# Performance work log

Hardware: AMD Instinct MI355X
Metric: run time of the kernel (lower is better)

The kernel has to match this reference:

```python
import jax, jax.numpy as jnp
import numpy as np

N_NODES = 100000
N_EDGES = 3200000
NUM_GRAPHS = 512
D_IN, D_H = 7, 16


def gcn_conv(x, edge_index, W, b, n_nodes):
    # PyG GCNConv: x' = D^{-1/2} (A + I) D^{-1/2} X W + b
    h = x @ W  # [N, d_out] -- do the tiny GEMM first (fewer bytes moved per edge)
    row, col = edge_index[0], edge_index[1]  # messages flow row -> col
    loop = jnp.arange(n_nodes)
    row = jnp.concatenate([row, loop])
    col = jnp.concatenate([col, loop])
    deg = jax.ops.segment_sum(jnp.ones(row.shape[0], dtype=h.dtype), col,
                              num_segments=n_nodes)
    dinv = jnp.where(deg > 0, jax.lax.rsqrt(deg), 0.0)
    norm = dinv[row] * dinv[col]                      # [E+N]
    msg = h[row] * norm[:, None]                      # gather + scale
    out = jax.ops.segment_sum(msg, col, num_segments=n_nodes)  # scatter-add
    return out + b


def setup_inputs() -> dict:
    key = jax.random.key(0)
    ks = jax.random.split(key, 9)
    x = jax.random.normal(ks[0], (N_NODES, D_IN), dtype=jnp.float32)
    edge_index = jax.random.randint(ks[1], (2, N_EDGES), 0, N_NODES, dtype=jnp.int64)
    batch = jnp.sort(jax.random.randint(ks[2], (N_NODES,), 0, NUM_GRAPHS, dtype=jnp.int64))
    def glorot(k, fan_in, fan_out):
        lim = np.sqrt(6.0 / (fan_in + fan_out)).astype(np.float32)
        return jax.random.uniform(k, (fan_in, fan_out), jnp.float32, -lim, lim)
    return {
        "x": x, "edge_index": edge_index, "batch": batch,
        "W1": glorot(ks[3], D_IN, D_H), "b1": jnp.zeros((D_H,), jnp.float32),
        "W2": glorot(ks[4], D_H, D_H), "b2": jnp.zeros((D_H,), jnp.float32),
        "Wl": glorot(ks[5], D_H, 1),   "bl": jnp.zeros((1,), jnp.float32),
    }


def reference(x, edge_index, batch, W1, b1, W2, b2, Wl, bl):
    n = x.shape[0]
    h = jax.nn.relu(gcn_conv(x, edge_index, W1, b1, n))
    h = jax.nn.relu(gcn_conv(h, edge_index, W2, b2, n))
    # global_mean_pool over graphs
    sums = jax.ops.segment_sum(h, batch, num_segments=NUM_GRAPHS)
    cnts = jax.ops.segment_sum(jnp.ones((n,), h.dtype), batch, num_segments=NUM_GRAPHS)
    pooled = sums / jnp.maximum(cnts, 1.0)[:, None]   # [G, 16]
    out = jax.nn.sigmoid(pooled @ Wl + bl)            # [G, 1]
    return out.squeeze(1)                             # [G]
```

## Files before the change

kernel.cpp:

```cpp
#include <hip/hip_runtime.h>
#include <hip/hip_fp16.h>
#include <math.h>

#define N_NODES    100000
#define N_EDGES    3200000
#define NUM_GRAPHS 512
#define D_IN       7
#define D_H        16
#define D_H2       8
#define SHIFT      7
#define BWIDTH     128
#define NB         782
#define CHUNK      8192
#define NCH        391
#define PC         2
#define PB         2
#define TPH        36
#define HST        (8 * TPH)
#define TP1        36
#define HST1       (4 * TP1)

__global__ void hist_kernel(const int* __restrict__ col, int* __restrict__ cnt) {
    __shared__ int lh[NB];
    int tid = threadIdx.x;
    for (int i = tid; i < NB; i += blockDim.x) lh[i] = 0;
    __syncthreads();
    int e0 = blockIdx.x * CHUNK;
    int e1 = e0 + CHUNK; if (e1 > N_EDGES) e1 = N_EDGES;
    for (int e = e0 + tid; e < e1; e += blockDim.x)
        atomicAdd(&lh[col[e] >> SHIFT], 1);
    __syncthreads();
    int* outp = cnt + (size_t)blockIdx.x * NB;
    for (int i = tid; i < NB; i += blockDim.x) outp[i] = lh[i];
}

__global__ void colscan_kernel(const int* __restrict__ cnt, int* __restrict__ base,
                               int* __restrict__ bcnt) {
    __shared__ int ts[256];
    int b = blockIdx.x;
    int tid = threadIdx.x;
    int c0 = tid * PC;
    int vals[PC];
    int sum = 0;
#pragma unroll
    for (int q = 0; q < PC; ++q) {
        int c = c0 + q;
        int v = (c < NCH) ? cnt[(size_t)c * NB + b] : 0;
        vals[q] = v; sum += v;
    }
    ts[tid] = sum;
    __syncthreads();
    for (int st = 1; st < 256; st <<= 1) {
        int v = (tid >= st) ? ts[tid - st] : 0;
        __syncthreads();
        ts[tid] += v;
        __syncthreads();
    }
    int run = ts[tid] - sum;
    int* bp = base + (size_t)b * NCH;
#pragma unroll
    for (int q = 0; q < PC; ++q) {
        int c = c0 + q;
        if (c < NCH) { bp[c] = run; run += vals[q]; }
    }
    if (tid == 0) bcnt[b] = ts[255];
}

__global__ void scan_kernel(const int* __restrict__ bcnt, int* __restrict__ offs) {
    __shared__ int lds[1024];
    int tid = threadIdx.x;
    lds[tid] = (tid < NB) ? bcnt[tid] : 0;
    __syncthreads();
    for (int st = 1; st < 1024; st <<= 1) {
        int v = (tid >= st) ? lds[tid - st] : 0;
        __syncthreads();
        lds[tid] += v;
        __syncthreads();
    }
    if (tid < NB) offs[tid + 1] = lds[tid];
    if (tid == 0) offs[0] = 0;
}

__global__ void place_kernel(const int* __restrict__ row, const int* __restrict__ col,
                             const int* __restrict__ base, const int* __restrict__ offs,
                             int* __restrict__ part) {
    __shared__ int lh[NB];
    __shared__ int sc[NB];
    __shared__ int lb[NB];
    __shared__ int ts[512];
    __shared__ int stage[CHUNK];
    __shared__ int dstv[CHUNK];

    int c = blockIdx.x;
    int tid = threadIdx.x;
    int e0 = c * CHUNK;
    int e1 = e0 + CHUNK; if (e1 > N_EDGES) e1 = N_EDGES;
    int n  = e1 - e0;

    for (int i = tid; i < NB; i += blockDim.x) lh[i] = 0;
    __syncthreads();
    for (int e = e0 + tid; e < e1; e += blockDim.x)
        atomicAdd(&lh[col[e] >> SHIFT], 1);
    __syncthreads();
    int b0 = tid * PB;
    int vals[PB];
    int sum = 0;
#pragma unroll
    for (int q = 0; q < PB; ++q) {
        int b = b0 + q;
        int v = (b < NB) ? lh[b] : 0;
        vals[q] = v; sum += v;
    }
    ts[tid] = sum;
    __syncthreads();
    for (int st = 1; st < 512; st <<= 1) {
        int v = (tid >= st) ? ts[tid - st] : 0;
        __syncthreads();
        ts[tid] += v;
        __syncthreads();
    }
    int run = ts[tid] - sum;
#pragma unroll
    for (int q = 0; q < PB; ++q) {
        int b = b0 + q;
        if (b < NB) {
            sc[b] = run;
            lb[b] = offs[b] + base[(size_t)b * NCH + c];
            run += vals[q];
            lh[b] = 0;
        }
    }
    __syncthreads();
    for (int e = e0 + tid; e < e1; e += blockDim.x) {
        int cc = col[e];
        int b = cc >> SHIFT;
        int rank = atomicAdd(&lh[b], 1);
        int loc = sc[b] + rank;
        stage[loc] = (row[e] << SHIFT) | (cc & (BWIDTH - 1));
        dstv[loc]  = lb[b] + rank;
    }
    __syncthreads();
    for (int i = tid; i < n; i += blockDim.x)
        part[dstv[i]] = stage[i];
}

__global__ void csr_kernel(const int* __restrict__ part, const int* __restrict__ offs,
                           const float* __restrict__ x,
                           int* __restrict__ csr, int* __restrict__ node_off,
                           int* __restrict__ deg, float* __restrict__ dinv,
                           unsigned* __restrict__ xsh) {
    __shared__ int cnt[BWIDTH];
    __shared__ int scn[BWIDTH];
    __shared__ int cur[BWIDTH];
    int b = blockIdx.x;
    int o0 = offs[b], o1 = offs[b + 1];
    if (threadIdx.x < BWIDTH) cnt[threadIdx.x] = 0;
    __syncthreads();
    for (int j = o0 + threadIdx.x; j < o1; j += blockDim.x)
        atomicAdd(&cnt[part[j] & (BWIDTH - 1)], 1);
    __syncthreads();
    if (threadIdx.x < BWIDTH) scn[threadIdx.x] = cnt[threadIdx.x];
    __syncthreads();
    for (int st = 1; st < BWIDTH; st <<= 1) {
        int v = 0;
        if (threadIdx.x < BWIDTH && threadIdx.x >= st) v = scn[threadIdx.x - st];
        __syncthreads();
        if (threadIdx.x < BWIDTH) scn[threadIdx.x] += v;
        __syncthreads();
    }
    if (threadIdx.x < BWIDTH) {
        int excl = scn[threadIdx.x] - cnt[threadIdx.x];
        cur[threadIdx.x] = excl;
        int c = b * BWIDTH + threadIdx.x;
        if (c < N_NODES) {
            node_off[c] = o0 + excl;
            deg[c] = cnt[threadIdx.x];
            float dv = rsqrtf((float)cnt[threadIdx.x] + 1.0f);
            dinv[c] = dv;
            float xv[8];
#pragma unroll
            for (int j = 0; j < D_IN; ++j) xv[j] = x[(size_t)c * D_IN + j] * dv;
            xv[7] = 0.f;
#pragma unroll
            for (int w = 0; w < 4; ++w) {
                __half2 p = __floats2half2_rn(xv[2 * w], xv[2 * w + 1]);
                xsh[(size_t)c * 4 + w] = *(unsigned*)&p;
            }
        }
    }
    __syncthreads();
    for (int j = o0 + threadIdx.x; j < o1; j += blockDim.x) {
        int e = part[j];
        int l = e & (BWIDTH - 1);
        int pos = atomicAdd(&cur[l], 1);
        csr[o0 + pos] = e >> SHIFT;
    }
}

__global__ void __launch_bounds__(256, 8)
pull1_kernel(const unsigned* __restrict__ xsh, const int* __restrict__ csr,
             const int* __restrict__ node_off, const int* __restrict__ deg,
             const float* __restrict__ dinv, const float* __restrict__ b1,
             const float* __restrict__ W1, const float* __restrict__ W2,
             unsigned* __restrict__ s2h) {
    __shared__ unsigned stage[4][2 * HST1];
    __shared__ float aggrow[4][2][8];
    __shared__ float hrow[4][2][D_H];
    int wave = threadIdx.x >> 6;
    int lane = threadIdx.x & 63;
    int h = lane >> 5, l = lane & 31;
    int v = blockIdx.x * 8 + wave * 2 + h;
    int k = l & 15;
    float w1c[D_IN];
#pragma unroll
    for (int j = 0; j < D_IN; ++j) w1c[j] = W1[j * D_H + k];
    float w2c[D_H];
#pragma unroll
    for (int j = 0; j < D_H; ++j) w2c[j] = W2[j * D_H + k];
    int d = deg[v], o0 = node_off[v];
    unsigned* stg = stage[wave] + h * HST1;
    int rg = l >> 3, p = l & 7;
    int w = p >> 1;
    bool hi = (p & 1);
    const uint4* rp = (const uint4*)(stg + w * TP1 + rg * 8);
    float acc = 0.f;
    for (int base = 0; base < d; base += 32) {
        int j = base + l;
        uint4 a = make_uint4(0u, 0u, 0u, 0u);
        if (j < d) {
            int r = __builtin_nontemporal_load(&csr[o0 + j]);
            a = *(const uint4*)(xsh + (size_t)r * 4);
        }
        asm volatile("s_waitcnt lgkmcnt(0)" ::: "memory");
        stg[0 * TP1 + l] = a.x;
        stg[1 * TP1 + l] = a.y;
        stg[2 * TP1 + l] = a.z;
        stg[3 * TP1 + l] = a.w;
        asm volatile("s_waitcnt lgkmcnt(0)" ::: "memory");
        uint4 q0 = rp[0], q1 = rp[1];
        unsigned ws[8] = { q0.x, q0.y, q0.z, q0.w, q1.x, q1.y, q1.z, q1.w };
#pragma unroll
        for (int i = 0; i < 8; ++i) {
            __half2 ph = *(__half2*)&ws[i];
            acc += hi ? __high2float(ph) : __low2float(ph);
        }
    }
    acc += __shfl_xor(acc, 8, 64);
    acc += __shfl_xor(acc, 16, 64);
    float dv = dinv[v];
    if (l < 8) aggrow[wave][h][l] = acc;
    asm volatile("s_waitcnt lgkmcnt(0)" ::: "memory");
    uint4 sx = *(const uint4*)(xsh + (size_t)v * 4);
    unsigned sxw[4] = { sx.x, sx.y, sx.z, sx.w };
    const float* ag = aggrow[wave][h];
    float hv = b1[k];
#pragma unroll
    for (int j = 0; j < D_IN; ++j) {
        __half2 ph = *(__half2*)&sxw[j >> 1];
        float xsv = (j & 1) ? __high2float(ph) : __low2float(ph);
        hv += dv * (ag[j] + xsv) * w1c[j];
    }
    hv = fmaxf(hv, 0.f);
    if (l < 16) hrow[wave][h][k] = hv;
    asm volatile("s_waitcnt lgkmcnt(0)" ::: "memory");
    const float4* hp = (const float4*)hrow[wave][h];
    float4 h0 = hp[0], h1 = hp[1], h2 = hp[2], h3 = hp[3];
    float a2 = h0.x * w2c[0] + h0.y * w2c[1] + h0.z * w2c[2] + h0.w * w2c[3]
             + h1.x * w2c[4] + h1.y * w2c[5] + h1.z * w2c[6] + h1.w * w2c[7]
             + h2.x * w2c[8] + h2.y * w2c[9] + h2.z * w2c[10] + h2.w * w2c[11]
             + h3.x * w2c[12] + h3.y * w2c[13] + h3.z * w2c[14] + h3.w * w2c[15];
    a2 *= dv;
    float a2hi = __shfl_xor(a2, 1, 64);
    if (l < 16 && (k & 1) == 0) {
        __half2 pq = __floats2half2_rn(a2, a2hi);
        s2h[(size_t)v * D_H2 + (k >> 1)] = *(unsigned*)&pq;
    }
}

__device__ __forceinline__ float gather_half(const unsigned* __restrict__ sh,
                                             const int* __restrict__ csr,
                                             int o0, int d, unsigned* stg, int l) {
    int g = l >> 4, k = l & 15;
    const uint4* rp = (const uint4*)(stg + (k >> 1) * TPH + g * 16);
    bool hi = (k & 1);
    float acc = 0.f;
    for (int base = 0; base < d; base += 32) {
        int j = base + l;
        uint4 a = make_uint4(0u, 0u, 0u, 0u), b = make_uint4(0u, 0u, 0u, 0u);
        if (j < d) {
            int r = __builtin_nontemporal_load(&csr[o0 + j]);
            const uint4* sp = (const uint4*)(sh + (size_t)r * D_H2);
            a = sp[0];
            b = sp[1];
        }
        asm volatile("s_waitcnt lgkmcnt(0)" ::: "memory");
        stg[0 * TPH + l] = a.x;
        stg[1 * TPH + l] = a.y;
        stg[2 * TPH + l] = a.z;
        stg[3 * TPH + l] = a.w;
        stg[4 * TPH + l] = b.x;
        stg[5 * TPH + l] = b.y;
        stg[6 * TPH + l] = b.z;
        stg[7 * TPH + l] = b.w;
        asm volatile("s_waitcnt lgkmcnt(0)" ::: "memory");
        uint4 q0 = rp[0], q1 = rp[1], q2 = rp[2], q3 = rp[3];
        unsigned ws[16] = { q0.x, q0.y, q0.z, q0.w, q1.x, q1.y, q1.z, q1.w,
                            q2.x, q2.y, q2.z, q2.w, q3.x, q3.y, q3.z, q3.w };
#pragma unroll
        for (int i = 0; i < 16; ++i) {
            __half2 p = *(__half2*)&ws[i];
            acc += hi ? __high2float(p) : __low2float(p);
        }
    }
    acc += __shfl_xor(acc, 16, 64);
    return acc;
}

__global__ void __launch_bounds__(256, 8)
pull2_kernel(const unsigned* __restrict__ sh, const int* __restrict__ csr,
             const int* __restrict__ node_off, const int* __restrict__ deg,
             const float* __restrict__ dinv, const float* __restrict__ b2,
             float* __restrict__ h2) {
    __shared__ unsigned stage[4][2 * HST];
    int wave = threadIdx.x >> 6;
    int lane = threadIdx.x & 63;
    int h = lane >> 5, l = lane & 31;
    int v = blockIdx.x * 8 + wave * 2 + h;
    int k = l & 15;
    int d = deg[v], o0 = node_off[v];
    unsigned* stg = stage[wave] + h * HST;
    float acc = gather_half(sh, csr, o0, d, stg, l);
    if (l < 16) {
        float dv = dinv[v];
        unsigned ws = sh[(size_t)v * D_H2 + (k >> 1)];
        __half2 ps = *(__half2*)&ws;
        float selfv = (k & 1) ? __high2float(ps) : __low2float(ps);
        float o = dv * (acc + selfv) + b2[k];
        h2[(size_t)v * D_H + k] = fmaxf(o, 0.f);
    }
}

__global__ void pool_head_kernel(const float* __restrict__ h, const int* __restrict__ batch,
                                 const float* __restrict__ Wl, const float* __restrict__ bl,
                                 float* __restrict__ out) {
    int g = blockIdx.x;
    int lo = 0, hi = N_NODES;
    while (lo < hi) { int m = (lo + hi) >> 1; if (batch[m] < g) lo = m + 1; else hi = m; }
    int v0 = lo;
    int lo2 = v0, hi2 = N_NODES;
    while (lo2 < hi2) { int m = (lo2 + hi2) >> 1; if (batch[m] < g + 1) lo2 = m + 1; else hi2 = m; }
    int v1 = lo2;
    int k = threadIdx.x & 15;
    int vi = threadIdx.x >> 4;
    float acc = 0.f;
    for (int v = v0 + vi; v < v1; v += 16) acc += h[v * D_H + k];
    acc += __shfl_xor(acc, 16, 64);
    acc += __shfl_xor(acc, 32, 64);
    __shared__ float sm[4][D_H];
    int lane = threadIdx.x & 63;
    if (lane < 16) sm[threadIdx.x >> 6][k] = acc;
    __syncthreads();
    if (threadIdx.x < 16) {
        float tot = sm[0][k] + sm[1][k] + sm[2][k] + sm[3][k];
        float cntf = (float)(v1 - v0);
        tot /= fmaxf(cntf, 1.0f);
        float p = tot * Wl[k];
        p += __shfl_xor(p, 1, 64);
        p += __shfl_xor(p, 2, 64);
        p += __shfl_xor(p, 4, 64);
        p += __shfl_xor(p, 8, 64);
        if (k == 0) out[g] = 1.0f / (1.0f + expf(-(p + bl[0])));
    }
}


extern "C" void kernel_launch(void* const* d_in, const int* in_sizes, int n_in,
                              void* d_out, int out_size, void* d_ws, size_t ws_size,
                              hipStream_t stream) {
    const float* x     = (const float*)d_in[0];
    const int*   ei    = (const int*)d_in[1];
    const int*   batch = (const int*)d_in[2];
    const float* W1    = (const float*)d_in[3];
    const float* b1    = (const float*)d_in[4];
    const float* W2    = (const float*)d_in[5];
    const float* b2    = (const float*)d_in[6];
    const float* Wl    = (const float*)d_in[7];
    const float* bl    = (const float*)d_in[8];
    float* out = (float*)d_out;

    const int* row = ei;
    const int* col = ei + N_EDGES;

    char* wsb = (char*)d_ws;
    size_t o = 0;
    int*      part     = (int*)(wsb + o);      o += (size_t)N_EDGES * 4;
    char*     regionA  = wsb + o;              o += (size_t)N_EDGES * 4;
    int*      cnt      = (int*)regionA;
    int*      base     = (int*)(regionA + (size_t)NCH * NB * 4);
    int*      csr      = (int*)regionA;
    int*      bcnt     = (int*)(wsb + o);      o += 1024 * 4;
    int*      offs     = (int*)(wsb + o);      o += 1024 * 4;
    int*      node_off = (int*)(wsb + o);      o += 100352 * 4;
    int*      deg      = (int*)(wsb + o);      o += 100352 * 4;
    float*    dinv     = (float*)(wsb + o);    o += 100352 * 4;
    unsigned* xsh      = (unsigned*)(wsb + o); o += (size_t)N_NODES * 4 * 4;
    unsigned* sBh      = (unsigned*)(wsb + o); o += (size_t)N_NODES * D_H2 * 4;
    float*    h2       = (float*)(wsb + o);    o += (size_t)N_NODES * D_H * 4;

    const int B = 256;

    hist_kernel<<<NCH, 512, 0, stream>>>(col, cnt);
    colscan_kernel<<<NB, B, 0, stream>>>(cnt, base, bcnt);
    scan_kernel<<<1, 1024, 0, stream>>>(bcnt, offs);
    place_kernel<<<NCH, 512, 0, stream>>>(row, col, base, offs, part);
    csr_kernel<<<NB, 512, 0, stream>>>(part, offs, x, csr, node_off, deg, dinv, xsh);

    pull1_kernel<<<N_NODES / 8, B, 0, stream>>>(xsh, csr, node_off, deg, dinv,
                                                b1, W1, W2, sBh);
    pull2_kernel<<<N_NODES / 8, B, 0, stream>>>(sBh, csr, node_off, deg, dinv,
                                                b2, h2);
    pool_head_kernel<<<NUM_GRAPHS, B, 0, stream>>>(h2, batch, Wl, bl, out);
}
```

Before: 134.9 us.

## Sort nodes by degree, prefetch next edge batch, vectorize edge index loads

Adds a degree histogram and a counting-sort permutation so the pull kernels process nodes grouped by similar degree, which evens out the per-wave work. Both pull kernels now software-prefetch the next 32-edge batch of neighbor features while the current batch is staged and reduced, hiding gather latency. The hist and place kernels read col/row as int4 vectors, which assumes the edge count is divisible by 4 per chunk. Costs are two extra small kernels, a memset, and more register pressure from the prefetch.

```diff
diff --git a/kernel.cpp b/kernel.cpp
--- a/kernel.cpp
+++ b/kernel.cpp
@@ -26,9 +26,16 @@
     for (int i = tid; i < NB; i += blockDim.x) lh[i] = 0;
     __syncthreads();
     int e0 = blockIdx.x * CHUNK;
-    int e1 = e0 + CHUNK; if (e1 > N_EDGES) e1 = N_EDGES;
-    for (int e = e0 + tid; e < e1; e += blockDim.x)
-        atomicAdd(&lh[col[e] >> SHIFT], 1);
+    int n  = N_EDGES - e0; if (n > CHUNK) n = CHUNK;
+    const int4* cp = (const int4*)(col + e0);
+    int n4 = n >> 2;
+    for (int q = tid; q < n4; q += blockDim.x) {
+        int4 v = cp[q];
+        atomicAdd(&lh[v.x >> SHIFT], 1);
+        atomicAdd(&lh[v.y >> SHIFT], 1);
+        atomicAdd(&lh[v.z >> SHIFT], 1);
+        atomicAdd(&lh[v.w >> SHIFT], 1);
+    }
     __syncthreads();
     int* outp = cnt + (size_t)blockIdx.x * NB;
     for (int i = tid; i < NB; i += blockDim.x) outp[i] = lh[i];
@@ -94,13 +101,20 @@
     int c = blockIdx.x;
     int tid = threadIdx.x;
     int e0 = c * CHUNK;
-    int e1 = e0 + CHUNK; if (e1 > N_EDGES) e1 = N_EDGES;
-    int n  = e1 - e0;
+    int n  = N_EDGES - e0; if (n > CHUNK) n = CHUNK;
+    int n4 = n >> 2;
+    const int4* cp = (const int4*)(col + e0);
+    const int4* rp = (const int4*)(row + e0);
 
     for (int i = tid; i < NB; i += blockDim.x) lh[i] = 0;
     __syncthreads();
-    for (int e = e0 + tid; e < e1; e += blockDim.x)
-        atomicAdd(&lh[col[e] >> SHIFT], 1);
+    for (int q = tid; q < n4; q += blockDim.x) {
+        int4 v = cp[q];
+        atomicAdd(&lh[v.x >> SHIFT], 1);
+        atomicAdd(&lh[v.y >> SHIFT], 1);
+        atomicAdd(&lh[v.z >> SHIFT], 1);
+        atomicAdd(&lh[v.w >> SHIFT], 1);
+    }
     __syncthreads();
     int b0 = tid * PB;
     int vals[PB];
@@ -131,13 +145,20 @@
         }
     }
     __syncthreads();
-    for (int e = e0 + tid; e < e1; e += blockDim.x) {
-        int cc = col[e];
-        int b = cc >> SHIFT;
-        int rank = atomicAdd(&lh[b], 1);
-        int loc = sc[b] + rank;
-        stage[loc] = (row[e] << SHIFT) | (cc & (BWIDTH - 1));
-        dstv[loc]  = lb[b] + rank;
+    for (int q = tid; q < n4; q += blockDim.x) {
+        int4 cc4 = cp[q];
+        int4 rr4 = rp[q];
+        int ccs[4] = { cc4.x, cc4.y, cc4.z, cc4.w };
+        int rrs[4] = { rr4.x, rr4.y, rr4.z, rr4.w };
+#pragma unroll
+        for (int t = 0; t < 4; ++t) {
+            int cc = ccs[t];
+            int b = cc >> SHIFT;
+            int rank = atomicAdd(&lh[b], 1);
+            int loc = sc[b] + rank;
+            stage[loc] = (rrs[t] << SHIFT) | (cc & (BWIDTH - 1));
+            dstv[loc]  = lb[b] + rank;
+        }
     }
     __syncthreads();
     for (int i = tid; i < n; i += blockDim.x)
@@ -148,13 +169,14 @@
                            const float* __restrict__ x,
                            int* __restrict__ csr, int* __restrict__ node_off,
                            int* __restrict__ deg, float* __restrict__ dinv,
-                           unsigned* __restrict__ xsh) {
+                           unsigned* __restrict__ xsh, int* __restrict__ dcnt) {
     __shared__ int cnt[BWIDTH];
     __shared__ int scn[BWIDTH];
     __shared__ int cur[BWIDTH];
+    __shared__ int dh[128];
     int b = blockIdx.x;
     int o0 = offs[b], o1 = offs[b + 1];
-    if (threadIdx.x < BWIDTH) cnt[threadIdx.x] = 0;
+    if (threadIdx.x < BWIDTH) { cnt[threadIdx.x] = 0; dh[threadIdx.x] = 0; }
     __syncthreads();
     for (int j = o0 + threadIdx.x; j < o1; j += blockDim.x)
         atomicAdd(&cnt[part[j] & (BWIDTH - 1)], 1);
@@ -175,6 +197,8 @@
         if (c < N_NODES) {
             node_off[c] = o0 + excl;
             deg[c] = cnt[threadIdx.x];
+            int bin = cnt[threadIdx.x]; if (bin > 127) bin = 127;
+            atomicAdd(&dh[bin], 1);
             float dv = rsqrtf((float)cnt[threadIdx.x] + 1.0f);
             dinv[c] = dv;
             float xv[8];
@@ -189,6 +213,7 @@
         }
     }
     __syncthreads();
+    if (threadIdx.x < 128 && dh[threadIdx.x]) atomicAdd(&dcnt[threadIdx.x], dh[threadIdx.x]);
     for (int j = o0 + threadIdx.x; j < o1; j += blockDim.x) {
         int e = part[j];
         int l = e & (BWIDTH - 1);
@@ -197,19 +222,52 @@
     }
 }
 
+__global__ void dscan_kernel(const int* __restrict__ dcnt, int* __restrict__ dcur) {
+    __shared__ int s[128];
+    int t = threadIdx.x;
+    s[t] = dcnt[t];
+    __syncthreads();
+    for (int st = 1; st < 128; st <<= 1) {
+        int v = (t >= st) ? s[t - st] : 0;
+        __syncthreads();
+        s[t] += v;
+        __syncthreads();
+    }
+    dcur[t] = s[t] - dcnt[t];
+}
+
+__global__ void dperm_kernel(const int* __restrict__ deg, int* __restrict__ dcur,
+                             int* __restrict__ perm) {
+    __shared__ int lh[128];
+    __shared__ int lb[128];
+    int tid = threadIdx.x;
+    if (tid < 128) lh[tid] = 0;
+    __syncthreads();
+    int v = blockIdx.x * 512 + tid;
+    int bin = 0, rank = 0;
+    if (v < N_NODES) {
+        bin = deg[v]; if (bin > 127) bin = 127;
+        rank = atomicAdd(&lh[bin], 1);
+    }
+    __syncthreads();
+    if (tid < 128) lb[tid] = lh[tid] ? atomicAdd(&dcur[tid], lh[tid]) : 0;
+    __syncthreads();
+    if (v < N_NODES) perm[lb[bin] + rank] = v;
+}
+
 __global__ void __launch_bounds__(256, 8)
 pull1_kernel(const unsigned* __restrict__ xsh, const int* __restrict__ csr,
              const int* __restrict__ node_off, const int* __restrict__ deg,
              const float* __restrict__ dinv, const float* __restrict__ b1,
              const float* __restrict__ W1, const float* __restrict__ W2,
-             unsigned* __restrict__ s2h) {
+             const int* __restrict__ perm, unsigned* __restrict__ s2h) {
     __shared__ unsigned stage[4][2 * HST1];
     __shared__ float aggrow[4][2][8];
     __shared__ float hrow[4][2][D_H];
     int wave = threadIdx.x >> 6;
     int lane = threadIdx.x & 63;
     int h = lane >> 5, l = lane & 31;
-    int v = blockIdx.x * 8 + wave * 2 + h;
+    int v = perm[blockIdx.x * 8 + wave * 2 + h];
     int k = l & 15;
     float w1c[D_IN];
 #pragma unroll
@@ -224,12 +282,17 @@
     bool hi = (p & 1);
     const uint4* rp = (const uint4*)(stg + w * TP1 + rg * 8);
     float acc = 0.f;
+    uint4 a = make_uint4(0u, 0u, 0u, 0u);
+    if (l < d) {
+        int r = __builtin_nontemporal_load(&csr[o0 + l]);
+        a = *(const uint4*)(xsh + (size_t)r * 4);
+    }
     for (int base = 0; base < d; base += 32) {
-        int j = base + l;
-        uint4 a = make_uint4(0u, 0u, 0u, 0u);
-        if (j < d) {
-            int r = __builtin_nontemporal_load(&csr[o0 + j]);
-            a = *(const uint4*)(xsh + (size_t)r * 4);
+        uint4 an = make_uint4(0u, 0u, 0u, 0u);
+        int jn = base + 32 + l;
+        if (jn < d) {
+            int r = __builtin_nontemporal_load(&csr[o0 + jn]);
+            an = *(const uint4*)(xsh + (size_t)r * 4);
         }
         asm volatile("s_waitcnt lgkmcnt(0)" ::: "memory");
         stg[0 * TP1 + l] = a.x;
@@ -244,6 +307,7 @@
             __half2 ph = *(__half2*)&ws[i];
             acc += hi ? __high2float(ph) : __low2float(ph);
         }
+        a = an;
     }
     acc += __shfl_xor(acc, 8, 64);
     acc += __shfl_xor(acc, 16, 64);
@@ -277,21 +341,38 @@
     }
 }
 
-__device__ __forceinline__ float gather_half(const unsigned* __restrict__ sh,
-                                             const int* __restrict__ csr,
-                                             int o0, int d, unsigned* stg, int l) {
-    int g = l >> 4, k = l & 15;
+__global__ void __launch_bounds__(256, 8)
+pull2_kernel(const unsigned* __restrict__ sh, const int* __restrict__ csr,
+             const int* __restrict__ node_off, const int* __restrict__ deg,
+             const float* __restrict__ dinv, const float* __restrict__ b2,
+             const int* __restrict__ perm, float* __restrict__ h2) {
+    __shared__ unsigned stage[4][2 * HST];
+    int wave = threadIdx.x >> 6;
+    int lane = threadIdx.x & 63;
+    int h = lane >> 5, l = lane & 31;
+    int v = perm[blockIdx.x * 8 + wave * 2 + h];
+    int k = l & 15;
+    int d = deg[v], o0 = node_off[v];
+    unsigned* stg = stage[wave] + h * HST;
+    int g = l >> 4;
     const uint4* rp = (const uint4*)(stg + (k >> 1) * TPH + g * 16);
     bool hi = (k & 1);
     float acc = 0.f;
+    uint4 a = make_uint4(0u, 0u, 0u, 0u), b = make_uint4(0u, 0u, 0u, 0u);
+    if (l < d) {
+        int r = __builtin_nontemporal_load(&csr[o0 + l]);
+        const uint4* sp = (const uint4*)(sh + (size_t)r * D_H2);
+        a = sp[0];
+        b = sp[1];
+    }
     for (int base = 0; base < d; base += 32) {
-        int j = base + l;
-        uint4 a = make_uint4(0u, 0u, 0u, 0u), b = make_uint4(0u, 0u, 0u, 0u);
-        if (j < d) {
-            int r = __builtin_nontemporal_load(&csr[o0 + j]);
+        uint4 an = make_uint4(0u, 0u, 0u, 0u), bn = make_uint4(0u, 0u, 0u, 0u);
+        int jn = base + 32 + l;
+        if (jn < d) {
+            int r = __builtin_nontemporal_load(&csr[o0 + jn]);
             const uint4* sp = (const uint4*)(sh + (size_t)r * D_H2);
-            a = sp[0];
-            b = sp[1];
+            an = sp[0];
+            bn = sp[1];
         }
         asm volatile("s_waitcnt lgkmcnt(0)" ::: "memory");
         stg[0 * TPH + l] = a.x;
@@ -311,29 +392,13 @@
             __half2 p = *(__half2*)&ws[i];
             acc += hi ? __high2float(p) : __low2float(p);
         }
+        a = an; b = bn;
     }
     acc += __shfl_xor(acc, 16, 64);
-    return acc;
-}
-
-__global__ void __launch_bounds__(256, 8)
-pull2_kernel(const unsigned* __restrict__ sh, const int* __restrict__ csr,
-             const int* __restrict__ node_off, const int* __restrict__ deg,
-             const float* __restrict__ dinv, const float* __restrict__ b2,
-             float* __restrict__ h2) {
-    __shared__ unsigned stage[4][2 * HST];
-    int wave = threadIdx.x >> 6;
-    int lane = threadIdx.x & 63;
-    int h = lane >> 5, l = lane & 31;
-    int v = blockIdx.x * 8 + wave * 2 + h;
-    int k = l & 15;
-    int d = deg[v], o0 = node_off[v];
-    unsigned* stg = stage[wave] + h * HST;
-    float acc = gather_half(sh, csr, o0, d, stg, l);
     if (l < 16) {
         float dv = dinv[v];
-        unsigned ws = sh[(size_t)v * D_H2 + (k >> 1)];
-        __half2 ps = *(__half2*)&ws;
+        unsigned wsv = sh[(size_t)v * D_H2 + (k >> 1)];
+        __half2 ps = *(__half2*)&wsv;
         float selfv = (k & 1) ? __high2float(ps) : __low2float(ps);
         float o = dv * (acc + selfv) + b2[k];
         h2[(size_t)v * D_H + k] = fmaxf(o, 0.f);
@@ -406,18 +471,26 @@
     unsigned* xsh      = (unsigned*)(wsb + o); o += (size_t)N_NODES * 4 * 4;
     unsigned* sBh      = (unsigned*)(wsb + o); o += (size_t)N_NODES * D_H2 * 4;
     float*    h2       = (float*)(wsb + o);    o += (size_t)N_NODES * D_H * 4;
+    int*      dcnt     = (int*)(wsb + o);      o += 128 * 4;
+    int*      dcur     = (int*)(wsb + o);      o += 128 * 4;
+    int*      perm     = (int*)(wsb + o);      o += 100352 * 4;
 
     const int B = 256;
 
+    hipMemsetAsync(dcnt, 0, 128 * sizeof(int), stream);
     hist_kernel<<<NCH, 512, 0, stream>>>(col, cnt);
     colscan_kernel<<<NB, B, 0, stream>>>(cnt, base, bcnt);
     scan_kernel<<<1, 1024, 0, stream>>>(bcnt, offs);
     place_kernel<<<NCH, 512, 0, stream>>>(row, col, base, offs, part);
-    csr_kernel<<<NB, 512, 0, stream>>>(part, offs, x, csr, node_off, deg, dinv, xsh);
+    csr_kernel<<<NB, 512, 0, stream>>>(part, offs, x, csr, node_off, deg, dinv,
+                                       xsh, dcnt);
+
+    dscan_kernel<<<1, 128, 0, stream>>>(dcnt, dcur);
+    dperm_kernel<<<(N_NODES + 511) / 512, 512, 0, stream>>>(deg, dcur, perm);
 
     pull1_kernel<<<N_NODES / 8, B, 0, stream>>>(xsh, csr, node_off, deg, dinv,
-                                                b1, W1, W2, sBh);
+                                                b1, W1, W2, perm, sBh);
     pull2_kernel<<<N_NODES / 8, B, 0, stream>>>(sBh, csr, node_off, deg, dinv,
-                                                b2, h2);
+                                                b2, perm, h2);
     pool_head_kernel<<<NUM_GRAPHS, B, 0, stream>>>(h2, batch, Wl, bl, out);
 }
```

Result: slower. 151.0 us (+11.9%).
